# Kernel optimization log

Measured on AMD Instinct MI355X. Metric: run time of the kernel, lower is better.

Reference implementation:

```python
import jax, jax.numpy as jnp
import numpy as np
import math

N_HEAD = 16
D_MODEL = 1024
ATT_DIM = D_MODEL // N_HEAD


def setup_inputs() -> dict:
    key = jax.random.key(0)
    ks = jax.random.split(key, 11)
    B, T, D = 2, 2048, D_MODEL
    s = 1.0 / math.sqrt(D)
    return {
        "q": jax.random.normal(ks[0], (B, T, D), jnp.float32),
        "k": jax.random.normal(ks[1], (B, T, D), jnp.float32),
        "v": jax.random.normal(ks[2], (B, T, D), jnp.float32),
        "Wq": jax.random.normal(ks[3], (D, D), jnp.float32) * s,
        "bq": jnp.zeros((D,), jnp.float32),
        "Wk": jax.random.normal(ks[4], (D, D), jnp.float32) * s,
        "bk": jnp.zeros((D,), jnp.float32),
        "Wv": jax.random.normal(ks[5], (D, D), jnp.float32) * s,
        "bv": jnp.zeros((D,), jnp.float32),
        "Wo": jax.random.normal(ks[6], (D, D), jnp.float32) * s,
        "bo": jnp.zeros((D,), jnp.float32),
    }


def reference(q, k, v, Wq, bq, Wk, bk, Wv, bv, Wo, bo):
    B, T, D = q.shape
    H, hd = N_HEAD, ATT_DIM
    # Linear projections (torch Linear: x @ W.T + b)
    qh = (q @ Wq.T + bq).reshape(B, T, H, hd).transpose(0, 2, 1, 3)  # [B,H,T,hd]
    kh = (k @ Wk.T + bk).reshape(B, T, H, hd).transpose(0, 2, 1, 3)
    vh = (v @ Wv.T + bv).reshape(B, T, H, hd).transpose(0, 2, 1, 3)
    scale = 1.0 / math.sqrt(hd)
    score = jnp.einsum("bhqd,bhkd->bhqk", qh, kh) * scale  # [B,H,T,T]
    attn = jax.nn.softmax(score, axis=-1)
    out = jnp.einsum("bhqk,bhkd->bhqd", attn, vh)  # [B,H,T,hd]
    out = out.transpose(0, 2, 1, 3).reshape(B, T, D)
    return out @ Wo.T + bo
```

## Files before the change

### kernel.cpp

```cpp
#include <hip/hip_runtime.h>


typedef __attribute__((ext_vector_type(8))) short bf16x8;
typedef __attribute__((ext_vector_type(4))) float f32x4;
typedef __attribute__((ext_vector_type(4))) unsigned int u32x4;
typedef __attribute__((ext_vector_type(2))) unsigned long long u64x2;

#define E22 ((size_t)1 << 22)
#define E20 ((size_t)1 << 20)

__device__ __forceinline__ unsigned short f2bf(float x) {
    unsigned int u = __float_as_uint(x);
    u += 0x7fffu + ((u >> 16) & 1u);
    return (unsigned short)(u >> 16);
}
__device__ __forceinline__ unsigned int pk2bf(float a, float b) {
    return __builtin_amdgcn_perm(__float_as_uint(a), __float_as_uint(b), 0x03020706u);
}
__device__ __forceinline__ void gl16(const void* g, void* l) {
    __builtin_amdgcn_global_load_lds(
        (const __attribute__((address_space(1))) void*)g,
        (__attribute__((address_space(3))) void*)l, 16, 0, 0);
}
__device__ __forceinline__ f32x4 mfma16(bf16x8 a, bf16x8 b, f32x4 c) {
    return __builtin_amdgcn_mfma_f32_16x16x32_bf16(a, b, c, 0, 0, 0);
}

__global__ __launch_bounds__(256)
void split_all(const float* __restrict__ q, const float* __restrict__ k,
               const float* __restrict__ v, const float* __restrict__ wq,
               const float* __restrict__ wk, const float* __restrict__ wv,
               const float* __restrict__ wo, unsigned short* __restrict__ ws)
{
    const size_t t = (size_t)blockIdx.x * 256 + threadIdx.x;
    const size_t e = t * 4;
    const float* src; unsigned short* dst; size_t off;
    if (e < 3 * E22) {
        const unsigned int which = (unsigned int)(e >> 22);
        src = which == 0 ? q : (which == 1 ? k : v);
        off = e & (E22 - 1);
        dst = ws + (size_t)which * E22;
    } else {
        const size_t e2 = e - 3 * E22;
        const unsigned int which = (unsigned int)(e2 >> 20);
        off = e2 & (E20 - 1);
        src = which == 0 ? wq : (which == 1 ? wk : (which == 2 ? wv : wo));
        dst = ws + 3 * E22 + (size_t)which * E20;
    }
    const float4 xv = *(const float4*)(src + off);
    ushort4 h4;
    h4.x = f2bf(xv.x); h4.y = f2bf(xv.y); h4.z = f2bf(xv.z); h4.w = f2bf(xv.w);
    *(ushort4*)(dst + off) = h4;
}

__global__ __launch_bounds__(256)
void gemm_qkv(const unsigned short* __restrict__ Xall,
              const unsigned short* __restrict__ Wcat,
              const float* __restrict__ bq, const float* __restrict__ bk,
              const float* __restrict__ bv, unsigned short* __restrict__ Qhp,
              unsigned short* __restrict__ Khp, unsigned short* __restrict__ Vtp)
{
    __shared__ unsigned short Xs[3 * 4096], Ws[3 * 4096];
    const int tid = threadIdx.x;
    const int w = tid >> 6, ln = tid & 63;
    const int quad = ln >> 4, L = ln & 15;
    const int wy = w >> 1, wx = w & 1;

    const int bid = blockIdx.x;
    const int xcd = bid & 7, j = bid >> 3;
    const int gg = xcd * 12 + (j >> 3);
    const int which = gg >> 5, m_i = gg & 31, n_i = j & 7;
    const int m0 = m_i * 128;

    const unsigned short* X = Xall + (size_t)which * E22;
    const unsigned short* W = Wcat + ((size_t)which * 1024 + n_i * 128) * 1024;
    const float* bp = which == 0 ? bq : (which == 1 ? bk : bv);
    unsigned short* outp = which == 0 ? Qhp : (which == 1 ? Khp : Vtp);
    const float qscale = which == 0 ? 0.18033688011f : 1.0f;

    const int ci0 = ln, ci1 = 64 + ln;
    const int row0 = w * 32 + (ci0 >> 2), row1 = w * 32 + (ci1 >> 2);
    const int gc0 = (ci0 & 3) ^ ((row0 >> 1) & 3);
    const int gc1 = (ci1 & 3) ^ ((row1 >> 1) & 3);
    const int lb0 = w * 2048, lb1 = w * 2048 + 1024;
    const unsigned short* Xbp = X + (size_t)m0 * 1024;
    const size_t gx0 = (size_t)row0 * 1024 + gc0 * 8;
    const size_t gx1 = (size_t)row1 * 1024 + gc1 * 8;

    f32x4 acc[4][4];
#pragma unroll
    for (int i = 0; i < 4; ++i)
#pragma unroll
        for (int jj = 0; jj < 4; ++jj) { f32x4 z = {0.f,0.f,0.f,0.f}; acc[i][jj] = z; }

#define QSTAGE(k0_, bo_)                                                       \
    do {                                                                       \
        gl16(Xbp + gx0 + (k0_), (char*)Xs + (bo_) + lb0);                      \
        gl16(W   + gx0 + (k0_), (char*)Ws + (bo_) + lb0);                      \
        gl16(Xbp + gx1 + (k0_), (char*)Xs + (bo_) + lb1);                      \
        gl16(W   + gx1 + (k0_), (char*)Ws + (bo_) + lb1);                      \
    } while (0)

#define QCOMP(eo_)                                                             \
    do {                                                                       \
        const unsigned short* Xc = Xs + (eo_);                                 \
        const unsigned short* Wc = Ws + (eo_);                                 \
        bf16x8 ah[4], bh[4];                                                   \
        _Pragma("unroll")                                                      \
        for (int mt = 0; mt < 4; ++mt) {                                       \
            const int row = wy * 64 + mt * 16 + L;                             \
            ah[mt] = *(const bf16x8*)(Xc + row * 32 +                          \
                                      ((quad ^ ((row >> 1) & 3)) * 8));        \
        }                                                                      \
        _Pragma("unroll")                                                      \
        for (int nt = 0; nt < 4; ++nt) {                                       \
            const int row = wx * 64 + nt * 16 + L;                             \
            bh[nt] = *(const bf16x8*)(Wc + row * 32 +                          \
                                      ((quad ^ ((row >> 1) & 3)) * 8));        \
        }                                                                      \
        _Pragma("unroll")                                                      \
        for (int mt = 0; mt < 4; ++mt)                                         \
            _Pragma("unroll")                                                  \
            for (int nt = 0; nt < 4; ++nt)                                     \
                acc[mt][nt] = mfma16(ah[mt], bh[nt], acc[mt][nt]);             \
    } while (0)

    QSTAGE(0, 0);
    QSTAGE(32, 8192);

    int cur = 0;
    for (int kt = 0; kt < 31; ++kt) {
        asm volatile("s_waitcnt vmcnt(4)" ::: "memory");
        __builtin_amdgcn_s_barrier();
        asm volatile("" ::: "memory");
        if (kt < 30) {
            int st = cur + 2; if (st >= 3) st -= 3;
            QSTAGE((kt + 2) * 32, st * 8192);
        }
        QCOMP(cur * 4096);
        cur = (cur == 2) ? 0 : cur + 1;
    }
    asm volatile("s_waitcnt vmcnt(0)" ::: "memory");
    __builtin_amdgcn_s_barrier();
    asm volatile("" ::: "memory");
    QCOMP(cur * 4096);
#undef QSTAGE
#undef QCOMP

#pragma unroll
    for (int mt = 0; mt < 4; ++mt)
#pragma unroll
        for (int nt = 0; nt < 4; ++nt) {
            const int gm0 = m0 + wy * 64 + mt * 16 + quad * 4;
            const int bn  = n_i * 128 + wx * 64 + nt * 16 + L;
            const float bvv = bp[bn];
            const int hh = bn >> 6, dd = bn & 63;
            if (which < 2) {
#pragma unroll
                for (int r = 0; r < 4; ++r) {
                    const int gm = gm0 + r;
                    const int bb = gm >> 11, tt = gm & 2047;
                    outp[((size_t)(bb * 16 + hh) * 2048 + tt) * 64 + dd] =
                        f2bf((acc[mt][nt][r] + bvv) * qscale);
                }
            } else {
                const int bb = gm0 >> 11, t0 = gm0 & 2047;
                ushort4 pk;
                pk.x = f2bf(acc[mt][nt][0] + bvv);
                pk.y = f2bf(acc[mt][nt][1] + bvv);
                pk.z = f2bf(acc[mt][nt][2] + bvv);
                pk.w = f2bf(acc[mt][nt][3] + bvv);
                *(ushort4*)(outp + ((size_t)(bb * 16 + hh) * 64 + dd) * 2048 + t0) = pk;
            }
        }
}

__global__ __launch_bounds__(256)
void gemm_out(const unsigned short* __restrict__ X, const unsigned short* __restrict__ W,
              const float* __restrict__ bias, float* __restrict__ outp)
{
    __shared__ unsigned short Xs[3 * 4096], Ws[3 * 2048];
    const int tid = threadIdx.x;
    const int w = tid >> 6, ln = tid & 63;
    const int quad = ln >> 4, L = ln & 15;

    const int bid = blockIdx.x;
    const int xcd = bid & 7, j = bid >> 3;
    const int m0 = (xcd * 4 + (j >> 4)) * 128;
    const int n0 = (j & 15) * 64;

    const int cix0 = ln, cix1 = 64 + ln;
    const int rowx0 = w * 32 + (cix0 >> 2), rowx1 = w * 32 + (cix1 >> 2);
    const int gcx0 = (cix0 & 3) ^ ((rowx0 >> 1) & 3);
    const int gcx1 = (cix1 & 3) ^ ((rowx1 >> 1) & 3);
    const int roww = w * 16 + (ln >> 2);
    const int gcw = (ln & 3) ^ ((roww >> 1) & 3);
    const size_t gxx0 = (size_t)(m0 + rowx0) * 1024 + gcx0 * 8;
    const size_t gxx1 = (size_t)(m0 + rowx1) * 1024 + gcx1 * 8;
    const size_t gww  = (size_t)(n0 + roww) * 1024 + gcw * 8;

    f32x4 acc[2][4];
#pragma unroll
    for (int i = 0; i < 2; ++i)
#pragma unroll
        for (int jj = 0; jj < 4; ++jj) { f32x4 z = {0.f,0.f,0.f,0.f}; acc[i][jj] = z; }

#define OSTAGE(k0_, bf_)                                                       \
    do {                                                                       \
        gl16(X + gxx0 + (k0_), (char*)Xs + (bf_) * 8192 + w * 2048);           \
        gl16(X + gxx1 + (k0_), (char*)Xs + (bf_) * 8192 + w * 2048 + 1024);    \
        gl16(W + gww  + (k0_), (char*)Ws + (bf_) * 4096 + w * 1024);           \
    } while (0)

#define OCOMP(bf_)                                                             \
    do {                                                                       \
        const unsigned short* Xc = Xs + (bf_) * 4096;                          \
        const unsigned short* Wc = Ws + (bf_) * 2048;                          \
        bf16x8 ah[2], bh[4];                                                   \
        _Pragma("unroll")                                                      \
        for (int mt = 0; mt < 2; ++mt) {                                       \
            const int row = w * 32 + mt * 16 + L;                              \
            ah[mt] = *(const bf16x8*)(Xc + row * 32 +                          \
                                      ((quad ^ ((row >> 1) & 3)) * 8));        \
        }                                                                      \
        _Pragma("unroll")                                                      \
        for (int nt = 0; nt < 4; ++nt) {                                       \
            const int row = nt * 16 + L;                                       \
            bh[nt] = *(const bf16x8*)(Wc + row * 32 +                          \
                                      ((quad ^ ((row >> 1) & 3)) * 8));        \
        }                                                                      \
        _Pragma("unroll")                                                      \
        for (int mt = 0; mt < 2; ++mt)                                         \
            _Pragma("unroll")                                                  \
            for (int nt = 0; nt < 4; ++nt)                                     \
                acc[mt][nt] = mfma16(ah[mt], bh[nt], acc[mt][nt]);             \
    } while (0)

    OSTAGE(0, 0);
    OSTAGE(32, 1);

    int cur = 0;
    for (int kt = 0; kt < 31; ++kt) {
        asm volatile("s_waitcnt vmcnt(3)" ::: "memory");
        __builtin_amdgcn_s_barrier();
        asm volatile("" ::: "memory");
        if (kt < 30) {
            int st = cur + 2; if (st >= 3) st -= 3;
            OSTAGE((kt + 2) * 32, st);
        }
        OCOMP(cur);
        cur = (cur == 2) ? 0 : cur + 1;
    }
    asm volatile("s_waitcnt vmcnt(0)" ::: "memory");
    __builtin_amdgcn_s_barrier();
    asm volatile("" ::: "memory");
    OCOMP(cur);
#undef OSTAGE
#undef OCOMP

#pragma unroll
    for (int mt = 0; mt < 2; ++mt)
#pragma unroll
        for (int nt = 0; nt < 4; ++nt) {
            const int gm0 = m0 + w * 32 + mt * 16 + quad * 4;
            const int gn  = n0 + nt * 16 + L;
            const float bvv = bias[gn];
#pragma unroll
            for (int r = 0; r < 4; ++r)
                outp[(size_t)(gm0 + r) * 1024 + gn] = acc[mt][nt][r] + bvv;
        }
}

__global__ __launch_bounds__(256, 2)
void flash(const unsigned short* __restrict__ Qh, const unsigned short* __restrict__ Kh,
           const unsigned short* __restrict__ Vt, unsigned short* __restrict__ A)
{
    __shared__ unsigned short KVs[16384];
    __shared__ float Lsc[2 * 4 * 64];
    const int tid = threadIdx.x;
    const int w = tid >> 6, ln = tid & 63;
    const int quad = ln >> 4, L = ln & 15;
    const int wq = w & 1, wk = w >> 1;

    const int bid = blockIdx.x;
    const int xcd = bid & 7, j = bid >> 3;
    const int bh_i = xcd * 4 + (j & 3);
    const int qt = j >> 2;
    const int b = bh_i >> 4, h = bh_i & 15;

    const unsigned short* Qb = Qh + ((size_t)bh_i * 2048 + qt * 128 + wq * 64) * 64;
    const unsigned short* Kb = Kh + (size_t)bh_i * 2048 * 64;
    const unsigned short* Vb = Vt + (size_t)bh_i * 64 * 2048;

    bf16x8 bq[4][2];
#pragma unroll
    for (int nt = 0; nt < 4; ++nt)
#pragma unroll
        for (int kc = 0; kc < 2; ++kc)
            bq[nt][kc] = *(const bf16x8*)(Qb + (nt * 16 + L) * 64 + kc * 32 + quad * 8);

    const short one_bf = (short)0x3F80;
    bf16x8 bone = {one_bf, one_bf, one_bf, one_bf, one_bf, one_bf, one_bf, one_bf};

    f32x4 o[4][4];
    f32x4 lacc[4];
#pragma unroll
    for (int mtd = 0; mtd < 4; ++mtd)
#pragma unroll
        for (int nt = 0; nt < 4; ++nt) { f32x4 z = {0.f,0.f,0.f,0.f}; o[mtd][nt] = z; }
#pragma unroll
    for (int nt = 0; nt < 4; ++nt) { f32x4 z = {0.f,0.f,0.f,0.f}; lacc[nt] = z; }

    const int ci0 = (w * 2 + 0) * 64 + ln, ci1 = (w * 2 + 1) * 64 + ln;
    const int rr0 = ci0 >> 3, rr1 = ci1 >> 3;
    const int gc0 = (ci0 & 7) ^ (rr0 & 7), gc1 = (ci1 & 7) ^ (rr1 & 7);

    const int rbv = L & 7;
    const int vg0 = ((wk * 4 + (quad >> 1)) ^ rbv) * 8 + (quad & 1) * 4;
    const int vg1 = ((wk * 4 + 2 + (quad >> 1)) ^ rbv) * 8 + (quad & 1) * 4;

#define STAGE(kt_, buf_)                                                        \
    do {                                                                        \
        gl16(Kb + (size_t)((kt_) * 64 + rr0) * 64 + gc0 * 8,                    \
             (char*)KVs + (buf_) * 8192 + (w * 2 + 0) * 1024);                  \
        gl16(Kb + (size_t)((kt_) * 64 + rr1) * 64 + gc1 * 8,                    \
             (char*)KVs + (buf_) * 8192 + (w * 2 + 1) * 1024);                  \
        gl16(Vb + (size_t)rr0 * 2048 + (kt_) * 64 + gc0 * 8,                    \
             (char*)KVs + 16384 + (buf_) * 8192 + (w * 2 + 0) * 1024);          \
        gl16(Vb + (size_t)rr1 * 2048 + (kt_) * 64 + gc1 * 8,                    \
             (char*)KVs + 16384 + (buf_) * 8192 + (w * 2 + 1) * 1024);          \
    } while (0)

    STAGE(0, 0);

    for (int kt = 0; kt < 32; ++kt) {
        const int cur = kt & 1;
        __syncthreads();
        if (kt < 31) STAGE(kt + 1, cur ^ 1);

        const unsigned short* Ksb = KVs + cur * 4096;
        const unsigned short* Vsb = KVs + 8192 + cur * 4096;

        bf16x8 ak[2][2];
#pragma unroll
        for (int mt = 0; mt < 2; ++mt)
#pragma unroll
            for (int kc = 0; kc < 2; ++kc) {
                const int row = wk * 32 + mt * 16 + L;
                ak[mt][kc] = *(const bf16x8*)(Ksb + row * 64 + (((kc * 4 + quad) ^ (L & 7)) * 8));
            }

        f32x4 s[2][4];
#pragma unroll
        for (int mt = 0; mt < 2; ++mt)
#pragma unroll
            for (int nt = 0; nt < 4; ++nt) {
                f32x4 z = {0.f,0.f,0.f,0.f};
                z = mfma16(ak[mt][0], bq[nt][0], z);
                z = mfma16(ak[mt][1], bq[nt][1], z);
                s[mt][nt] = z;
            }

        bf16x8 pbx[4];
#pragma unroll
        for (int nt = 0; nt < 4; ++nt) {
            u32x4 pd;
            pd.x = pk2bf(__builtin_amdgcn_exp2f(s[0][nt][0]),
                         __builtin_amdgcn_exp2f(s[0][nt][1]));
            pd.y = pk2bf(__builtin_amdgcn_exp2f(s[0][nt][2]),
                         __builtin_amdgcn_exp2f(s[0][nt][3]));
            pd.z = pk2bf(__builtin_amdgcn_exp2f(s[1][nt][0]),
                         __builtin_amdgcn_exp2f(s[1][nt][1]));
            pd.w = pk2bf(__builtin_amdgcn_exp2f(s[1][nt][2]),
                         __builtin_amdgcn_exp2f(s[1][nt][3]));
            pbx[nt] = __builtin_bit_cast(bf16x8, pd);
        }

        bf16x8 av[4];
#pragma unroll
        for (int mtd = 0; mtd < 4; ++mtd) {
            const unsigned short* Vr = Vsb + (mtd * 16 + L) * 64;
            u64x2 t;
            t.x = *(const unsigned long long*)(Vr + vg0);
            t.y = *(const unsigned long long*)(Vr + vg1);
            av[mtd] = __builtin_bit_cast(bf16x8, t);
        }

#pragma unroll
        for (int mtd = 0; mtd < 4; ++mtd)
#pragma unroll
            for (int nt = 0; nt < 4; ++nt)
                o[mtd][nt] = mfma16(av[mtd], pbx[nt], o[mtd][nt]);
#pragma unroll
        for (int nt = 0; nt < 4; ++nt)
            lacc[nt] = mfma16(bone, pbx[nt], lacc[nt]);
    }
#undef STAGE

    __syncthreads();
    float* Rb = (float*)KVs;
    if (wk == 1) {
#pragma unroll
        for (int mtd = 0; mtd < 4; ++mtd)
#pragma unroll
            for (int nt = 0; nt < 4; ++nt)
                *(f32x4*)(Rb + wq * 4096 + (mtd * 4 + nt) * 256 + ln * 4) = o[mtd][nt];
#pragma unroll
        for (int nt = 0; nt < 4; ++nt)
            Lsc[wq * 256 + nt * 64 + ln] = lacc[nt][0];
    }
    __syncthreads();
    if (wk == 0) {
#pragma unroll
        for (int mtd = 0; mtd < 4; ++mtd)
#pragma unroll
            for (int nt = 0; nt < 4; ++nt)
                o[mtd][nt] += *(const f32x4*)(Rb + wq * 4096 + (mtd * 4 + nt) * 256 + ln * 4);

#pragma unroll
        for (int nt = 0; nt < 4; ++nt) {
            const float lsum = lacc[nt][0] + Lsc[wq * 256 + nt * 64 + ln];
            const float inv = 1.0f / lsum;
            const int qrow = b * 2048 + qt * 128 + wq * 64 + nt * 16 + L;
#pragma unroll
            for (int mtd = 0; mtd < 4; ++mtd) {
                const int d0 = mtd * 16 + quad * 4;
                ushort4 pk;
                pk.x = f2bf(o[mtd][nt][0] * inv);
                pk.y = f2bf(o[mtd][nt][1] * inv);
                pk.z = f2bf(o[mtd][nt][2] * inv);
                pk.w = f2bf(o[mtd][nt][3] * inv);
                *(ushort4*)(A + (size_t)qrow * 1024 + h * 64 + d0) = pk;
            }
        }
    }
}

extern "C" void kernel_launch(void* const* d_in, const int* in_sizes, int n_in,
                              void* d_out, int out_size, void* d_ws, size_t ws_size,
                              hipStream_t stream) {
    const float* q  = (const float*)d_in[0];
    const float* k  = (const float*)d_in[1];
    const float* v  = (const float*)d_in[2];
    const float* Wq = (const float*)d_in[3];
    const float* bq = (const float*)d_in[4];
    const float* Wk = (const float*)d_in[5];
    const float* bk = (const float*)d_in[6];
    const float* Wv = (const float*)d_in[7];
    const float* bv = (const float*)d_in[8];
    const float* Wo = (const float*)d_in[9];
    const float* bo = (const float*)d_in[10];

    unsigned short* W = (unsigned short*)d_ws;
    unsigned short *Xall = W;
    unsigned short *Wcat = W + 3 * E22;
    unsigned short *Wob  = Wcat + 3 * E20;
    unsigned short *Qhp  = W + 4 * E22;
    unsigned short *Khp  = W + 5 * E22;
    unsigned short *Vtp  = W + 6 * E22;
    unsigned short *A    = W;

    split_all<<<16384, 256, 0, stream>>>(q, k, v, Wq, Wk, Wv, Wo, W);

    gemm_qkv<<<768, 256, 0, stream>>>(Xall, Wcat, bq, bk, bv, Qhp, Khp, Vtp);

    flash<<<512, 256, 0, stream>>>(Qhp, Khp, Vtp, A);

    gemm_out<<<512, 256, 0, stream>>>(A, Wob, bo, (float*)d_out);
}
```

Measured before the change: 212.4 us.

## Enlarge flash block to 8 waves with triple-buffered K/V and setprio

The flash attention kernel now runs 512-thread blocks covering 256 query rows, with half as many blocks, so each K/V tile staged in LDS serves twice as many query rows. The double-buffered K/V pipeline becomes a three-deep ring with explicit vmcnt waits and raw barriers, so loads run two tiles ahead. The MFMA sections are also wrapped in s_setprio. The aim is to cut global K/V traffic and hide load latency, at the cost of more LDS per block and a grid of only 256 blocks, which may leave parts of the chip less evenly loaded.

```diff
diff --git a/kernel.cpp b/kernel.cpp
--- a/kernel.cpp
+++ b/kernel.cpp
@@ -271,16 +271,16 @@
         }
 }
 
-__global__ __launch_bounds__(256, 2)
+__global__ __launch_bounds__(512, 2)
 void flash(const unsigned short* __restrict__ Qh, const unsigned short* __restrict__ Kh,
            const unsigned short* __restrict__ Vt, unsigned short* __restrict__ A)
 {
-    __shared__ unsigned short KVs[16384];
-    __shared__ float Lsc[2 * 4 * 64];
+    __shared__ unsigned short SM[32768];
+    __shared__ float Lsc[4 * 4 * 64];
     const int tid = threadIdx.x;
     const int w = tid >> 6, ln = tid & 63;
     const int quad = ln >> 4, L = ln & 15;
-    const int wq = w & 1, wk = w >> 1;
+    const int wq = w & 3, wk = w >> 2;
 
     const int bid = blockIdx.x;
     const int xcd = bid & 7, j = bid >> 3;
@@ -288,7 +288,7 @@
     const int qt = j >> 2;
     const int b = bh_i >> 4, h = bh_i & 15;
 
-    const unsigned short* Qb = Qh + ((size_t)bh_i * 2048 + qt * 128 + wq * 64) * 64;
+    const unsigned short* Qb = Qh + ((size_t)bh_i * 2048 + qt * 256 + wq * 64) * 64;
     const unsigned short* Kb = Kh + (size_t)bh_i * 2048 * 64;
     const unsigned short* Vb = Vt + (size_t)bh_i * 64 * 2048;
 
@@ -311,9 +311,9 @@
 #pragma unroll
     for (int nt = 0; nt < 4; ++nt) { f32x4 z = {0.f,0.f,0.f,0.f}; lacc[nt] = z; }
 
-    const int ci0 = (w * 2 + 0) * 64 + ln, ci1 = (w * 2 + 1) * 64 + ln;
-    const int rr0 = ci0 >> 3, rr1 = ci1 >> 3;
-    const int gc0 = (ci0 & 7) ^ (rr0 & 7), gc1 = (ci1 & 7) ^ (rr1 & 7);
+    const int ci = w * 64 + ln;
+    const int rr = ci >> 3;
+    const int gc = (ci & 7) ^ (rr & 7);
 
     const int rbv = L & 7;
     const int vg0 = ((wk * 4 + (quad >> 1)) ^ rbv) * 8 + (quad & 1) * 4;
@@ -321,25 +321,28 @@
 
 #define STAGE(kt_, buf_)                                                        \
     do {                                                                        \
-        gl16(Kb + (size_t)((kt_) * 64 + rr0) * 64 + gc0 * 8,                    \
-             (char*)KVs + (buf_) * 8192 + (w * 2 + 0) * 1024);                  \
-        gl16(Kb + (size_t)((kt_) * 64 + rr1) * 64 + gc1 * 8,                    \
-             (char*)KVs + (buf_) * 8192 + (w * 2 + 1) * 1024);                  \
-        gl16(Vb + (size_t)rr0 * 2048 + (kt_) * 64 + gc0 * 8,                    \
-             (char*)KVs + 16384 + (buf_) * 8192 + (w * 2 + 0) * 1024);          \
-        gl16(Vb + (size_t)rr1 * 2048 + (kt_) * 64 + gc1 * 8,                    \
-             (char*)KVs + 16384 + (buf_) * 8192 + (w * 2 + 1) * 1024);          \
+        gl16(Kb + (size_t)((kt_) * 64 + rr) * 64 + gc * 8,                      \
+             (char*)SM + (buf_) * 8192 + w * 1024);                             \
+        gl16(Vb + (size_t)rr * 2048 + (kt_) * 64 + gc * 8,                      \
+             (char*)SM + 24576 + (buf_) * 8192 + w * 1024);                     \
     } while (0)
 
     STAGE(0, 0);
-
+    STAGE(1, 1);
+
+    int cur = 0, st = 2;
     for (int kt = 0; kt < 32; ++kt) {
-        const int cur = kt & 1;
-        __syncthreads();
-        if (kt < 31) STAGE(kt + 1, cur ^ 1);
-
-        const unsigned short* Ksb = KVs + cur * 4096;
-        const unsigned short* Vsb = KVs + 8192 + cur * 4096;
+        if (kt < 31) {
+            asm volatile("s_waitcnt vmcnt(2)" ::: "memory");
+        } else {
+            asm volatile("s_waitcnt vmcnt(0)" ::: "memory");
+        }
+        __builtin_amdgcn_s_barrier();
+        asm volatile("" ::: "memory");
+        if (kt < 30) STAGE(kt + 2, st);
+
+        const unsigned short* Ksb = SM + cur * 4096;
+        const unsigned short* Vsb = SM + 12288 + cur * 4096;
 
         bf16x8 ak[2][2];
 #pragma unroll
@@ -351,6 +354,7 @@
             }
 
         f32x4 s[2][4];
+        __builtin_amdgcn_s_setprio(1);
 #pragma unroll
         for (int mt = 0; mt < 2; ++mt)
 #pragma unroll
@@ -360,6 +364,7 @@
                 z = mfma16(ak[mt][1], bq[nt][1], z);
                 s[mt][nt] = z;
             }
+        __builtin_amdgcn_s_setprio(0);
 
         bf16x8 pbx[4];
 #pragma unroll
@@ -386,6 +391,7 @@
             av[mtd] = __builtin_bit_cast(bf16x8, t);
         }
 
+        __builtin_amdgcn_s_setprio(1);
 #pragma unroll
         for (int mtd = 0; mtd < 4; ++mtd)
 #pragma unroll
@@ -394,11 +400,15 @@
 #pragma unroll
         for (int nt = 0; nt < 4; ++nt)
             lacc[nt] = mfma16(bone, pbx[nt], lacc[nt]);
+        __builtin_amdgcn_s_setprio(0);
+
+        cur = (cur == 2) ? 0 : cur + 1;
+        st  = (st  == 2) ? 0 : st  + 1;
     }
 #undef STAGE
 
     __syncthreads();
-    float* Rb = (float*)KVs;
+    float* Rb = (float*)SM;
     if (wk == 1) {
 #pragma unroll
         for (int mtd = 0; mtd < 4; ++mtd)
@@ -421,7 +431,7 @@
         for (int nt = 0; nt < 4; ++nt) {
             const float lsum = lacc[nt][0] + Lsc[wq * 256 + nt * 64 + ln];
             const float inv = 1.0f / lsum;
-            const int qrow = b * 2048 + qt * 128 + wq * 64 + nt * 16 + L;
+            const int qrow = b * 2048 + qt * 256 + wq * 64 + nt * 16 + L;
 #pragma unroll
             for (int mtd = 0; mtd < 4; ++mtd) {
                 const int d0 = mtd * 16 + quad * 4;
@@ -464,7 +474,7 @@
 
     gemm_qkv<<<768, 256, 0, stream>>>(Xall, Wcat, bq, bk, bv, Qhp, Khp, Vtp);
 
-    flash<<<512, 256, 0, stream>>>(Qhp, Khp, Vtp, A);
+    flash<<<256, 512, 0, stream>>>(Qhp, Khp, Vtp, A);
 
     gemm_out<<<512, 256, 0, stream>>>(A, Wob, bo, (float*)d_out);
 }
```

After: 219.0 us. 3.1% more time.

## Use per-wave private K staging with triple buffering and direct V register loads

Applied to the files above, without the earlier changes.

Each wave now stages only its own 32-key slice of K into a private triple-buffered LDS region and loads V straight from global memory into registers, with the loads issued one or two tiles ahead. Block-wide __syncthreads in the key loop are replaced by s_waitcnt vmcnt counters. The aim is to remove the barrier stalls and the LDS round trip for V, so loads overlap better with MFMA work. In exchange, V reads become strided, less coalesced global accesses, register pressure rises from the double-buffered V fragments, and LDS use grows, which may limit occupancy at two blocks per CU.

```diff
diff --git a/kernel.cpp b/kernel.cpp
--- a/kernel.cpp
+++ b/kernel.cpp
@@ -275,7 +275,7 @@
 void flash(const unsigned short* __restrict__ Qh, const unsigned short* __restrict__ Kh,
            const unsigned short* __restrict__ Vt, unsigned short* __restrict__ A)
 {
-    __shared__ unsigned short KVs[16384];
+    __shared__ unsigned short SM[24576];
     __shared__ float Lsc[2 * 4 * 64];
     const int tid = threadIdx.x;
     const int w = tid >> 6, ln = tid & 63;
@@ -289,8 +289,8 @@
     const int b = bh_i >> 4, h = bh_i & 15;
 
     const unsigned short* Qb = Qh + ((size_t)bh_i * 2048 + qt * 128 + wq * 64) * 64;
-    const unsigned short* Kb = Kh + (size_t)bh_i * 2048 * 64;
-    const unsigned short* Vb = Vt + (size_t)bh_i * 64 * 2048;
+    const unsigned short* Kb = Kh + ((size_t)bh_i * 2048 + wk * 32) * 64;
+    const unsigned short* Vb = Vt + (size_t)bh_i * 64 * 2048 + wk * 32;
 
     bf16x8 bq[4][2];
 #pragma unroll
@@ -311,94 +311,106 @@
 #pragma unroll
     for (int nt = 0; nt < 4; ++nt) { f32x4 z = {0.f,0.f,0.f,0.f}; lacc[nt] = z; }
 
-    const int ci0 = (w * 2 + 0) * 64 + ln, ci1 = (w * 2 + 1) * 64 + ln;
-    const int rr0 = ci0 >> 3, rr1 = ci1 >> 3;
-    const int gc0 = (ci0 & 7) ^ (rr0 & 7), gc1 = (ci1 & 7) ^ (rr1 & 7);
-
-    const int rbv = L & 7;
-    const int vg0 = ((wk * 4 + (quad >> 1)) ^ rbv) * 8 + (quad & 1) * 4;
-    const int vg1 = ((wk * 4 + 2 + (quad >> 1)) ^ rbv) * 8 + (quad & 1) * 4;
-
-#define STAGE(kt_, buf_)                                                        \
+    const int rl  = ln >> 3;
+    const int gck = (ln & 7) ^ rl;
+    char* Kw = (char*)SM + w * 12288;
+
+#define KSTAGE(kt_, bo_)                                                        \
     do {                                                                        \
-        gl16(Kb + (size_t)((kt_) * 64 + rr0) * 64 + gc0 * 8,                    \
-             (char*)KVs + (buf_) * 8192 + (w * 2 + 0) * 1024);                  \
-        gl16(Kb + (size_t)((kt_) * 64 + rr1) * 64 + gc1 * 8,                    \
-             (char*)KVs + (buf_) * 8192 + (w * 2 + 1) * 1024);                  \
-        gl16(Vb + (size_t)rr0 * 2048 + (kt_) * 64 + gc0 * 8,                    \
-             (char*)KVs + 16384 + (buf_) * 8192 + (w * 2 + 0) * 1024);          \
-        gl16(Vb + (size_t)rr1 * 2048 + (kt_) * 64 + gc1 * 8,                    \
-             (char*)KVs + 16384 + (buf_) * 8192 + (w * 2 + 1) * 1024);          \
-    } while (0)
-
-    STAGE(0, 0);
-
-    for (int kt = 0; kt < 32; ++kt) {
-        const int cur = kt & 1;
-        __syncthreads();
-        if (kt < 31) STAGE(kt + 1, cur ^ 1);
-
-        const unsigned short* Ksb = KVs + cur * 4096;
-        const unsigned short* Vsb = KVs + 8192 + cur * 4096;
-
-        bf16x8 ak[2][2];
-#pragma unroll
-        for (int mt = 0; mt < 2; ++mt)
-#pragma unroll
-            for (int kc = 0; kc < 2; ++kc) {
-                const int row = wk * 32 + mt * 16 + L;
-                ak[mt][kc] = *(const bf16x8*)(Ksb + row * 64 + (((kc * 4 + quad) ^ (L & 7)) * 8));
-            }
-
-        f32x4 s[2][4];
-#pragma unroll
-        for (int mt = 0; mt < 2; ++mt)
-#pragma unroll
-            for (int nt = 0; nt < 4; ++nt) {
-                f32x4 z = {0.f,0.f,0.f,0.f};
-                z = mfma16(ak[mt][0], bq[nt][0], z);
-                z = mfma16(ak[mt][1], bq[nt][1], z);
-                s[mt][nt] = z;
-            }
-
-        bf16x8 pbx[4];
-#pragma unroll
-        for (int nt = 0; nt < 4; ++nt) {
-            u32x4 pd;
-            pd.x = pk2bf(__builtin_amdgcn_exp2f(s[0][nt][0]),
-                         __builtin_amdgcn_exp2f(s[0][nt][1]));
-            pd.y = pk2bf(__builtin_amdgcn_exp2f(s[0][nt][2]),
-                         __builtin_amdgcn_exp2f(s[0][nt][3]));
-            pd.z = pk2bf(__builtin_amdgcn_exp2f(s[1][nt][0]),
-                         __builtin_amdgcn_exp2f(s[1][nt][1]));
-            pd.w = pk2bf(__builtin_amdgcn_exp2f(s[1][nt][2]),
-                         __builtin_amdgcn_exp2f(s[1][nt][3]));
-            pbx[nt] = __builtin_bit_cast(bf16x8, pd);
-        }
-
-        bf16x8 av[4];
-#pragma unroll
-        for (int mtd = 0; mtd < 4; ++mtd) {
-            const unsigned short* Vr = Vsb + (mtd * 16 + L) * 64;
-            u64x2 t;
-            t.x = *(const unsigned long long*)(Vr + vg0);
-            t.y = *(const unsigned long long*)(Vr + vg1);
-            av[mtd] = __builtin_bit_cast(bf16x8, t);
-        }
-
-#pragma unroll
-        for (int mtd = 0; mtd < 4; ++mtd)
-#pragma unroll
-            for (int nt = 0; nt < 4; ++nt)
-                o[mtd][nt] = mfma16(av[mtd], pbx[nt], o[mtd][nt]);
-#pragma unroll
-        for (int nt = 0; nt < 4; ++nt)
-            lacc[nt] = mfma16(bone, pbx[nt], lacc[nt]);
-    }
-#undef STAGE
+        _Pragma("unroll")                                                       \
+        for (int i_ = 0; i_ < 4; ++i_)                                          \
+            gl16(Kb + (size_t)((kt_) * 64 + i_ * 8 + rl) * 64 + gck * 8,        \
+                 Kw + (bo_) + i_ * 1024);                                       \
+    } while (0)
+
+#define VLOAD(kt_, dst_)                                                        \
+    do {                                                                        \
+        _Pragma("unroll")                                                       \
+        for (int m_ = 0; m_ < 4; ++m_) {                                        \
+            const unsigned short* Vr = Vb + (size_t)(m_ * 16 + L) * 2048 +      \
+                                       (kt_) * 64 + quad * 4;                   \
+            u64x2 t_;                                                           \
+            t_.x = *(const unsigned long long*)(Vr);                            \
+            t_.y = *(const unsigned long long*)(Vr + 16);                       \
+            dst_[m_] = __builtin_bit_cast(bf16x8, t_);                          \
+        }                                                                       \
+    } while (0)
+
+#define COMP(bo_, av_)                                                          \
+    do {                                                                        \
+        const char* Kc = Kw + (bo_);                                            \
+        bf16x8 ak[2][2];                                                        \
+        _Pragma("unroll")                                                       \
+        for (int mt = 0; mt < 2; ++mt)                                          \
+            _Pragma("unroll")                                                   \
+            for (int kc = 0; kc < 2; ++kc)                                      \
+                ak[mt][kc] = *(const bf16x8*)(Kc + (mt * 16 + L) * 128 +        \
+                                              (((kc * 4 + quad) ^ (L & 7)) * 16)); \
+        f32x4 s[2][4];                                                          \
+        _Pragma("unroll")                                                       \
+        for (int mt = 0; mt < 2; ++mt)                                          \
+            _Pragma("unroll")                                                   \
+            for (int nt = 0; nt < 4; ++nt) {                                    \
+                f32x4 z = {0.f, 0.f, 0.f, 0.f};                                 \
+                z = mfma16(ak[mt][0], bq[nt][0], z);                            \
+                z = mfma16(ak[mt][1], bq[nt][1], z);                            \
+                s[mt][nt] = z;                                                  \
+            }                                                                   \
+        bf16x8 pbx[4];                                                          \
+        _Pragma("unroll")                                                       \
+        for (int nt = 0; nt < 4; ++nt) {                                        \
+            u32x4 pd;                                                           \
+            pd.x = pk2bf(__builtin_amdgcn_exp2f(s[0][nt][0]),                   \
+                         __builtin_amdgcn_exp2f(s[0][nt][1]));                  \
+            pd.y = pk2bf(__builtin_amdgcn_exp2f(s[0][nt][2]),                   \
+                         __builtin_amdgcn_exp2f(s[0][nt][3]));                  \
+            pd.z = pk2bf(__builtin_amdgcn_exp2f(s[1][nt][0]),                   \
+                         __builtin_amdgcn_exp2f(s[1][nt][1]));                  \
+            pd.w = pk2bf(__builtin_amdgcn_exp2f(s[1][nt][2]),                   \
+                         __builtin_amdgcn_exp2f(s[1][nt][3]));                  \
+            pbx[nt] = __builtin_bit_cast(bf16x8, pd);                           \
+        }                                                                       \
+        _Pragma("unroll")                                                       \
+        for (int mtd = 0; mtd < 4; ++mtd)                                       \
+            _Pragma("unroll")                                                   \
+            for (int nt = 0; nt < 4; ++nt)                                      \
+                o[mtd][nt] = mfma16(av_[mtd], pbx[nt], o[mtd][nt]);             \
+        _Pragma("unroll")                                                       \
+        for (int nt = 0; nt < 4; ++nt)                                          \
+            lacc[nt] = mfma16(bone, pbx[nt], lacc[nt]);                         \
+    } while (0)
+
+    bf16x8 avA[4], avB[4];
+    VLOAD(0, avA); KSTAGE(0, 0);
+    VLOAD(1, avB); KSTAGE(1, 4096);
+
+    int bo = 0, bs = 8192;
+#pragma unroll 1
+    for (int kt = 0; kt < 30; kt += 2) {
+        asm volatile("s_waitcnt vmcnt(12)" ::: "memory");
+        COMP(bo, avA);
+        VLOAD(kt + 2, avA);
+        KSTAGE(kt + 2, bs);
+        bo = (bo == 8192) ? 0 : bo + 4096;
+        bs = (bs == 8192) ? 0 : bs + 4096;
+        asm volatile("s_waitcnt vmcnt(12)" ::: "memory");
+        COMP(bo, avB);
+        VLOAD(kt + 3, avB);
+        KSTAGE(kt + 3, bs);
+        bo = (bo == 8192) ? 0 : bo + 4096;
+        bs = (bs == 8192) ? 0 : bs + 4096;
+    }
+    asm volatile("s_waitcnt vmcnt(12)" ::: "memory");
+    COMP(bo, avA);
+    bo = (bo == 8192) ? 0 : bo + 4096;
+    asm volatile("s_waitcnt vmcnt(0)" ::: "memory");
+    COMP(bo, avB);
+#undef KSTAGE
+#undef VLOAD
+#undef COMP
 
     __syncthreads();
-    float* Rb = (float*)KVs;
+    float* Rb = (float*)SM;
     if (wk == 1) {
 #pragma unroll
         for (int mtd = 0; mtd < 4; ++mtd)
```

Measured after the change: 244.6 us. 15.2% more time.
